# Kernel tuning notes

Hardware: AMD Instinct MI355X
Metric: run time of the kernel (lower is better)

Reference implementation:

```python
import jax, jax.numpy as jnp
import numpy as np

B, T, D, F = 4, 2048, 2048, 8192
RANK = 16
ALPHA = 32.0
SCALING = ALPHA / RANK  # rslora=False -> alpha/rank = 2.0


def setup_inputs() -> dict:
    key = jax.random.key(0)
    k_x, k_w, k_a, k_b = jax.random.split(key, 4)
    x = jax.random.normal(k_x, (B, T, D), dtype=jnp.float32)
    # Main weight: real init_fn default is zeros; use randn for a meaningful baseline.
    w = jax.random.normal(k_w, (D, F), dtype=jnp.float32) * 0.02
    # LoRA factors: config.init_fn = normal(stddev=0.01)
    lora_a = jax.random.normal(k_a, (D, RANK), dtype=jnp.float32) * 0.01
    lora_b = jax.random.normal(k_b, (RANK, F), dtype=jnp.float32) * 0.01
    return {"x": x, "w": w, "lora_a": lora_a, "lora_b": lora_b}


def reference(x, w, lora_a, lora_b):
    # eqn:   btd,df->btf   (main GEMM)
    # eqn_a: btd,dL->btL   (LoRA down-projection, L = rank)
    # eqn_b: btL,Lf->btf   (LoRA up-projection)
    result = jnp.einsum('btd,df->btf', x, w.astype(x.dtype))
    lora = jnp.einsum('btd,dL->btL', x, lora_a.astype(x.dtype))
    lora = jnp.einsum('btL,Lf->btf', lora, lora_b.astype(x.dtype))
    return result + lora * SCALING
```

## Files before the change

kernel.cpp:

```cpp
#include <hip/hip_runtime.h>
#include <stdint.h>
#include <stddef.h>


typedef __bf16 bf16;
typedef __bf16 bf16x4 __attribute__((ext_vector_type(4)));
typedef __bf16 bf16x8 __attribute__((ext_vector_type(8)));
typedef float  f32x4  __attribute__((ext_vector_type(4)));

#define M_DIM 8192
#define N_DIM 8192
#define K_DIM 2048
#define LRANK 16
#define LSCALE 2.0f

#define BM 128
#define BN 128
#define BK 64

typedef __attribute__((address_space(1))) void* as1_void;
typedef __attribute__((address_space(3))) void* as3_void;

__device__ __forceinline__ void gload_lds16(const void* g, void* l) {
    __builtin_amdgcn_global_load_lds((as1_void)(g), (as3_void)(l), 16, 0, 0);
}

__global__ void convert_x_kernel(const float* __restrict__ x,
                                 bf16* __restrict__ xb) {
    int i = (blockIdx.x * blockDim.x + threadIdx.x) * 4;
    float4 v = *(const float4*)(x + i);
    bf16x4 o;
    o.x = (bf16)v.x; o.y = (bf16)v.y; o.z = (bf16)v.z; o.w = (bf16)v.w;
    *(bf16x4*)(xb + i) = o;
}

__global__ void fold_transpose_kernel(const float* __restrict__ w,
                                      const float* __restrict__ la,
                                      const float* __restrict__ lb,
                                      bf16* __restrict__ wt) {
    __shared__ float tile[32][33];
    __shared__ float at[32][17];
    __shared__ float bt[16][32];

    const int k0 = blockIdx.x * 32;
    const int n0 = blockIdx.y * 32;
    const int t  = threadIdx.x;
    const int c  = t & 31;
    const int r0 = t >> 5;

    #pragma unroll
    for (int rr = 0; rr < 32; rr += 8)
        tile[r0 + rr][c] = w[(size_t)(k0 + r0 + rr) * N_DIM + n0 + c];

    at[t >> 4][t & 15]          = la[(size_t)(k0 + (t >> 4)) * LRANK + (t & 15)];
    at[(t + 256) >> 4][t & 15]  = la[(size_t)(k0 + ((t + 256) >> 4)) * LRANK + (t & 15)];

    bt[t >> 5][c]       = lb[(size_t)(t >> 5) * N_DIM + n0 + c];
    bt[(t >> 5) + 8][c] = lb[(size_t)((t >> 5) + 8) * N_DIM + n0 + c];

    __syncthreads();

    #pragma unroll
    for (int rr = 0; rr < 32; rr += 8) {
        const int nl = r0 + rr;
        const int kl = c;
        float delta = 0.f;
        #pragma unroll
        for (int L = 0; L < LRANK; ++L)
            delta += at[kl][L] * bt[L][nl];
        float v = tile[kl][nl] + LSCALE * delta;
        wt[(size_t)(n0 + nl) * K_DIM + k0 + kl] = (bf16)v;
    }
}

__global__ __launch_bounds__(256)
void gemm_bf16_kernel(const bf16* __restrict__ A,
                      const bf16* __restrict__ Bt,
                      float* __restrict__ C) {
    __shared__ __align__(16) bf16 As[BM * BK];
    __shared__ __align__(16) bf16 Bs[BN * BK];

    const int t    = threadIdx.x;
    const int lane = t & 63;
    const int wave = t >> 6;
    const int wm   = (wave >> 1) * 64;
    const int wn   = (wave & 1) * 64;

    const int n0 = blockIdx.x * BN;
    const int m0 = blockIdx.y * BM;

    int rowS[4], clS[4];
    #pragma unroll
    for (int j = 0; j < 4; ++j) {
        int p   = j * 4096 + t * 16;
        int row = p >> 7;
        int cp  = (p >> 4) & 7;
        rowS[j] = row;
        clS[j]  = cp ^ (row & 7);
    }
    const bf16* aBase = A  + (size_t)m0 * K_DIM;
    const bf16* bBase = Bt + (size_t)n0 * K_DIM;

    int offA[2][4], offB[2][4];
    #pragma unroll
    for (int ks = 0; ks < 2; ++ks) {
        #pragma unroll
        for (int i = 0; i < 4; ++i) {
            int rowa = wm + i * 16 + (lane & 15);
            int rowb = wn + i * 16 + (lane & 15);
            int cl   = ks * 4 + (lane >> 4);
            offA[ks][i] = rowa * 64 + ((cl ^ (rowa & 7)) * 8);
            offB[ks][i] = rowb * 64 + ((cl ^ (rowb & 7)) * 8);
        }
    }

    f32x4 acc[4][4] = {};

    for (int kt = 0; kt < K_DIM / BK; ++kt) {
        const int k0 = kt * BK;
        #pragma unroll
        for (int j = 0; j < 4; ++j) {
            gload_lds16(aBase + (size_t)rowS[j] * K_DIM + k0 + clS[j] * 8,
                        As + j * 2048 + t * 8);
            gload_lds16(bBase + (size_t)rowS[j] * K_DIM + k0 + clS[j] * 8,
                        Bs + j * 2048 + t * 8);
        }
        __syncthreads();

        #pragma unroll
        for (int ks = 0; ks < 2; ++ks) {
            bf16x8 af[4], bfr[4];
            #pragma unroll
            for (int i = 0; i < 4; ++i) af[i]  = *(const bf16x8*)(As + offA[ks][i]);
            #pragma unroll
            for (int i = 0; i < 4; ++i) bfr[i] = *(const bf16x8*)(Bs + offB[ks][i]);
            #pragma unroll
            for (int mi = 0; mi < 4; ++mi)
                #pragma unroll
                for (int ni = 0; ni < 4; ++ni)
                    acc[mi][ni] = __builtin_amdgcn_mfma_f32_16x16x32_bf16(
                        af[mi], bfr[ni], acc[mi][ni], 0, 0, 0);
        }
        __syncthreads();
    }

    const int cr = (lane >> 4) * 4;
    const int cc = lane & 15;
    float* cBase = C + (size_t)(m0 + wm + cr) * N_DIM + (n0 + wn + cc);
    #pragma unroll
    for (int mi = 0; mi < 4; ++mi)
        #pragma unroll
        for (int r = 0; r < 4; ++r)
            #pragma unroll
            for (int ni = 0; ni < 4; ++ni)
                cBase[(size_t)(mi * 16 + r) * N_DIM + ni * 16] = acc[mi][ni][r];
}

extern "C" void kernel_launch(void* const* d_in, const int* in_sizes, int n_in,
                              void* d_out, int out_size, void* d_ws, size_t ws_size,
                              hipStream_t stream) {
    const float* x  = (const float*)d_in[0];
    const float* w  = (const float*)d_in[1];
    const float* la = (const float*)d_in[2];
    const float* lb = (const float*)d_in[3];
    float* out = (float*)d_out;

    bf16* xb = (bf16*)d_ws;
    bf16* wt = (bf16*)((char*)d_ws + (size_t)M_DIM * K_DIM * 2);

    convert_x_kernel<<<M_DIM * K_DIM / 4 / 256, 256, 0, stream>>>(x, xb);
    fold_transpose_kernel<<<dim3(K_DIM / 32, N_DIM / 32), 256, 0, stream>>>(w, la, lb, wt);
    gemm_bf16_kernel<<<dim3(N_DIM / BN, M_DIM / BM), 256, 0, stream>>>(xb, wt, out);
}
```

Baseline: 622.0 us.

## Use 32x32x16 MFMA in GEMM and widen preprocessing kernels

The GEMM inner loop switches from 16x16x32 to 32x32x16 bf16 MFMA with a 2x2 accumulator tile per wave, which cuts LDS fragment reads per MFMA and changes the epilogue store pattern. The x conversion kernel now handles 8 elements per thread with 16-byte stores. The fold/transpose kernel moves to 64x64 tiles with float4 loads, LoRA factors held in registers, and vectorized bf16x8 stores. Register pressure rises in the fold kernel, and the GEMM epilogue writes 32-wide rows per store.

```diff
diff --git a/kernel.cpp b/kernel.cpp
--- a/kernel.cpp
+++ b/kernel.cpp
@@ -4,9 +4,8 @@
 
 
 typedef __bf16 bf16;
-typedef __bf16 bf16x4 __attribute__((ext_vector_type(4)));
 typedef __bf16 bf16x8 __attribute__((ext_vector_type(8)));
-typedef float  f32x4  __attribute__((ext_vector_type(4)));
+typedef float  f32x16 __attribute__((ext_vector_type(16)));
 
 #define M_DIM 8192
 #define N_DIM 8192
@@ -27,49 +26,77 @@
 
 __global__ void convert_x_kernel(const float* __restrict__ x,
                                  bf16* __restrict__ xb) {
-    int i = (blockIdx.x * blockDim.x + threadIdx.x) * 4;
-    float4 v = *(const float4*)(x + i);
-    bf16x4 o;
-    o.x = (bf16)v.x; o.y = (bf16)v.y; o.z = (bf16)v.z; o.w = (bf16)v.w;
-    *(bf16x4*)(xb + i) = o;
+    size_t i = (size_t)(blockIdx.x * blockDim.x + threadIdx.x) * 8;
+    float4 v0 = *(const float4*)(x + i);
+    float4 v1 = *(const float4*)(x + i + 4);
+    bf16x8 o;
+    o[0] = (bf16)v0.x; o[1] = (bf16)v0.y; o[2] = (bf16)v0.z; o[3] = (bf16)v0.w;
+    o[4] = (bf16)v1.x; o[5] = (bf16)v1.y; o[6] = (bf16)v1.z; o[7] = (bf16)v1.w;
+    *(bf16x8*)(xb + i) = o;
 }
 
 __global__ void fold_transpose_kernel(const float* __restrict__ w,
                                       const float* __restrict__ la,
                                       const float* __restrict__ lb,
                                       bf16* __restrict__ wt) {
-    __shared__ float tile[32][33];
-    __shared__ float at[32][17];
-    __shared__ float bt[16][32];
-
-    const int k0 = blockIdx.x * 32;
-    const int n0 = blockIdx.y * 32;
+    __shared__ float tile[64][65];
+    __shared__ float at[64][17];
+    __shared__ float bt[16][64];
+
+    const int k0 = blockIdx.x * 64;
+    const int n0 = blockIdx.y * 64;
     const int t  = threadIdx.x;
-    const int c  = t & 31;
-    const int r0 = t >> 5;
-
-    #pragma unroll
-    for (int rr = 0; rr < 32; rr += 8)
-        tile[r0 + rr][c] = w[(size_t)(k0 + r0 + rr) * N_DIM + n0 + c];
-
-    at[t >> 4][t & 15]          = la[(size_t)(k0 + (t >> 4)) * LRANK + (t & 15)];
-    at[(t + 256) >> 4][t & 15]  = la[(size_t)(k0 + ((t + 256) >> 4)) * LRANK + (t & 15)];
-
-    bt[t >> 5][c]       = lb[(size_t)(t >> 5) * N_DIM + n0 + c];
-    bt[(t >> 5) + 8][c] = lb[(size_t)((t >> 5) + 8) * N_DIM + n0 + c];
-
+
+    {
+        const int r = t >> 4;
+        const int c4 = (t & 15) * 4;
+        #pragma unroll
+        for (int p = 0; p < 4; ++p) {
+            const int row = r + p * 16;
+            float4 v = *(const float4*)(w + (size_t)(k0 + row) * N_DIM + n0 + c4);
+            tile[row][c4 + 0] = v.x; tile[row][c4 + 1] = v.y;
+            tile[row][c4 + 2] = v.z; tile[row][c4 + 3] = v.w;
+        }
+    }
+    {
+        const int row = t >> 2, c4 = (t & 3) * 4;
+        float4 v = *(const float4*)(la + (size_t)(k0 + row) * LRANK + c4);
+        at[row][c4 + 0] = v.x; at[row][c4 + 1] = v.y;
+        at[row][c4 + 2] = v.z; at[row][c4 + 3] = v.w;
+    }
+    {
+        const int row = t >> 4, c4 = (t & 15) * 4;
+        float4 v = *(const float4*)(lb + (size_t)row * N_DIM + n0 + c4);
+        bt[row][c4 + 0] = v.x; bt[row][c4 + 1] = v.y;
+        bt[row][c4 + 2] = v.z; bt[row][c4 + 3] = v.w;
+    }
     __syncthreads();
 
-    #pragma unroll
-    for (int rr = 0; rr < 32; rr += 8) {
-        const int nl = r0 + rr;
-        const int kl = c;
-        float delta = 0.f;
+    const int kl0 = (t & 7) * 8;
+    const int nlb = t >> 3;
+
+    float areg[8][LRANK];
+    #pragma unroll
+    for (int j = 0; j < 8; ++j)
         #pragma unroll
         for (int L = 0; L < LRANK; ++L)
-            delta += at[kl][L] * bt[L][nl];
-        float v = tile[kl][nl] + LSCALE * delta;
-        wt[(size_t)(n0 + nl) * K_DIM + k0 + kl] = (bf16)v;
+            areg[j][L] = at[kl0 + j][L];
+
+    #pragma unroll
+    for (int h = 0; h < 2; ++h) {
+        const int nl = nlb + h * 32;
+        float bcol[LRANK];
+        #pragma unroll
+        for (int L = 0; L < LRANK; ++L) bcol[L] = bt[L][nl];
+        bf16x8 o;
+        #pragma unroll
+        for (int j = 0; j < 8; ++j) {
+            float delta = 0.f;
+            #pragma unroll
+            for (int L = 0; L < LRANK; ++L) delta += areg[j][L] * bcol[L];
+            o[j] = (bf16)(tile[kl0 + j][nl] + LSCALE * delta);
+        }
+        *(bf16x8*)(wt + (size_t)(n0 + nl) * K_DIM + k0 + kl0) = o;
     }
 }
 
@@ -101,20 +128,20 @@
     const bf16* aBase = A  + (size_t)m0 * K_DIM;
     const bf16* bBase = Bt + (size_t)n0 * K_DIM;
 
-    int offA[2][4], offB[2][4];
-    #pragma unroll
-    for (int ks = 0; ks < 2; ++ks) {
-        #pragma unroll
-        for (int i = 0; i < 4; ++i) {
-            int rowa = wm + i * 16 + (lane & 15);
-            int rowb = wn + i * 16 + (lane & 15);
-            int cl   = ks * 4 + (lane >> 4);
-            offA[ks][i] = rowa * 64 + ((cl ^ (rowa & 7)) * 8);
-            offB[ks][i] = rowb * 64 + ((cl ^ (rowb & 7)) * 8);
-        }
-    }
-
-    f32x4 acc[4][4] = {};
+    int offA[4][2], offB[4][2];
+    #pragma unroll
+    for (int s = 0; s < 4; ++s) {
+        const int cl = s * 2 + (lane >> 5);
+        #pragma unroll
+        for (int i = 0; i < 2; ++i) {
+            const int rowa = wm + i * 32 + (lane & 31);
+            const int rowb = wn + i * 32 + (lane & 31);
+            offA[s][i] = rowa * 64 + ((cl ^ (rowa & 7)) * 8);
+            offB[s][i] = rowb * 64 + ((cl ^ (rowb & 7)) * 8);
+        }
+    }
+
+    f32x16 acc[2][2] = {};
 
     for (int kt = 0; kt < K_DIM / BK; ++kt) {
         const int k0 = kt * BK;
@@ -128,32 +155,34 @@
         __syncthreads();
 
         #pragma unroll
-        for (int ks = 0; ks < 2; ++ks) {
-            bf16x8 af[4], bfr[4];
-            #pragma unroll
-            for (int i = 0; i < 4; ++i) af[i]  = *(const bf16x8*)(As + offA[ks][i]);
-            #pragma unroll
-            for (int i = 0; i < 4; ++i) bfr[i] = *(const bf16x8*)(Bs + offB[ks][i]);
-            #pragma unroll
-            for (int mi = 0; mi < 4; ++mi)
+        for (int s = 0; s < 4; ++s) {
+            bf16x8 af[2], bfr[2];
+            #pragma unroll
+            for (int i = 0; i < 2; ++i) af[i]  = *(const bf16x8*)(As + offA[s][i]);
+            #pragma unroll
+            for (int i = 0; i < 2; ++i) bfr[i] = *(const bf16x8*)(Bs + offB[s][i]);
+            #pragma unroll
+            for (int mi = 0; mi < 2; ++mi)
                 #pragma unroll
-                for (int ni = 0; ni < 4; ++ni)
-                    acc[mi][ni] = __builtin_amdgcn_mfma_f32_16x16x32_bf16(
+                for (int ni = 0; ni < 2; ++ni)
+                    acc[mi][ni] = __builtin_amdgcn_mfma_f32_32x32x16_bf16(
                         af[mi], bfr[ni], acc[mi][ni], 0, 0, 0);
         }
         __syncthreads();
     }
 
-    const int cr = (lane >> 4) * 4;
-    const int cc = lane & 15;
-    float* cBase = C + (size_t)(m0 + wm + cr) * N_DIM + (n0 + wn + cc);
-    #pragma unroll
-    for (int mi = 0; mi < 4; ++mi)
-        #pragma unroll
-        for (int r = 0; r < 4; ++r)
-            #pragma unroll
-            for (int ni = 0; ni < 4; ++ni)
-                cBase[(size_t)(mi * 16 + r) * N_DIM + ni * 16] = acc[mi][ni][r];
+    const int cc = lane & 31;
+    const int rb = 4 * (lane >> 5);
+    float* cBase = C + (size_t)(m0 + wm + rb) * N_DIM + (n0 + wn + cc);
+    #pragma unroll
+    for (int mi = 0; mi < 2; ++mi)
+        #pragma unroll
+        for (int ni = 0; ni < 2; ++ni)
+            #pragma unroll
+            for (int r = 0; r < 16; ++r) {
+                const int rowo = mi * 32 + (r & 3) + 8 * (r >> 2);
+                cBase[(size_t)rowo * N_DIM + ni * 32] = acc[mi][ni][r];
+            }
 }
 
 extern "C" void kernel_launch(void* const* d_in, const int* in_sizes, int n_in,
@@ -168,7 +197,7 @@
     bf16* xb = (bf16*)d_ws;
     bf16* wt = (bf16*)((char*)d_ws + (size_t)M_DIM * K_DIM * 2);
 
-    convert_x_kernel<<<M_DIM * K_DIM / 4 / 256, 256, 0, stream>>>(x, xb);
-    fold_transpose_kernel<<<dim3(K_DIM / 32, N_DIM / 32), 256, 0, stream>>>(w, la, lb, wt);
+    convert_x_kernel<<<M_DIM * K_DIM / 8 / 256, 256, 0, stream>>>(x, xb);
+    fold_transpose_kernel<<<dim3(K_DIM / 64, N_DIM / 64), 256, 0, stream>>>(w, la, lb, wt);
     gemm_bf16_kernel<<<dim3(N_DIM / BN, M_DIM / BM), 256, 0, stream>>>(xb, wt, out);
 }
```

New measurement: 753.5 us. 1.21x slower.
